# Kernel optimization log

Measured on AMD Instinct MI355X. Metric: run time of the kernel, lower is better.

Reference implementation:

```python
import jax, jax.numpy as jnp
import numpy as np

B, S, D, C = 1024, 200, 64, 256  # batch, max_seq_length_all, reshape_size, codebook_size


def setup_inputs() -> dict:
    key = jax.random.key(0)
    k1, k2, k3 = jax.random.split(key, 3)
    rq_item_embeddings = jax.random.normal(k1, (B, S, D), dtype=jnp.float32)
    labels = jax.random.randint(k2, (B, S), 0, C, dtype=jnp.int32)
    attention_mask = jax.random.randint(k3, (B, S), 0, 2, dtype=jnp.int32)
    return {
        "rq_item_embeddings": rq_item_embeddings,
        "labels": labels,
        "attention_mask": attention_mask,
    }


def reference(rq_item_embeddings, labels, attention_mask):
    # Batched version of the original per-sample loop:
    #   M[c, s] = 1 if labels[s] == c, masked by attention_mask[s]
    #   M <- L1-normalize over seq dim (divide each cluster row by its count)
    #   cluster_emb = M @ sample  (per-cluster mean of item embeddings)
    x = rq_item_embeddings  # [B, S, D]
    mask = attention_mask.astype(x.dtype)  # [B, S]
    # one-hot cluster assignment, [B, C, S]
    one_hot = (labels[:, None, :] == jnp.arange(C, dtype=labels.dtype)[None, :, None])
    cluster_mask = one_hot.astype(x.dtype) * mask[:, None, :]  # [B, C, S]
    counts = cluster_mask.sum(axis=-1)  # [B, C]  (== L1 norm of each row)
    inv = jnp.where(counts > 0, 1.0 / jnp.maximum(counts, 1.0), 0.0)  # [B, C]
    # normalized scatter matrix @ embeddings -> per-cluster mean, [B, C, D]
    cluster_emb = jnp.einsum('bcs,bsd->bcd', cluster_mask, x) * inv[:, :, None]
    return cluster_emb, cluster_mask.astype(jnp.int32)
```

## Files before the change

kernel.cpp:

```cpp
#include <hip/hip_runtime.h>

#define NB 1024
#define NS 200
#define ND 64
#define NC 256

typedef float v4f __attribute__((ext_vector_type(4)));

__global__ __launch_bounds__(256) void s3rec_mask_kernel(
    const int* __restrict__ labels,
    const int* __restrict__ amask,
    float* __restrict__ out_mask)
{
    __shared__ __align__(16) int s_lab[NS];

    const int bid = blockIdx.x;
    const int b   = bid >> 2;
    const int ct  = (bid & 3) << 6;
    const int t   = threadIdx.x;

    for (int i = t; i < NS; i += 256) {
        const int l = labels[b * NS + i];
        const int m = amask [b * NS + i];
        s_lab[i] = (m != 0) ? l : -1;
    }
    __syncthreads();

    const int4* lab4 = reinterpret_cast<const int4*>(s_lab);
    v4f* om4 = reinterpret_cast<v4f*>(out_mask + (size_t)b * (NC * NS)) + ct * 50;
    for (int i4 = t; i4 < 64 * 50; i4 += 256) {
        const int cl = i4 / 50;
        const int s4 = i4 - cl * 50;
        const int c  = ct + cl;
        const int4 L = lab4[s4];
        v4f v;
        v.x = (L.x == c) ? 1.0f : 0.0f;
        v.y = (L.y == c) ? 1.0f : 0.0f;
        v.z = (L.z == c) ? 1.0f : 0.0f;
        v.w = (L.w == c) ? 1.0f : 0.0f;
        om4[i4] = v;
    }
}

__global__ __launch_bounds__(256) void s3rec_emb_kernel(
    const float* __restrict__ x,
    const int*   __restrict__ labels,
    const int*   __restrict__ amask,
    float* __restrict__ out_emb)
{
    __shared__ __align__(16) float s_emb[NC * ND];
    __shared__ int   s_lab[NS];
    __shared__ float s_inv[NC];

    const int b = blockIdx.x;
    const int t = threadIdx.x;

    for (int i = t; i < NS; i += 256) {
        const int l = labels[b * NS + i];
        const int m = amask [b * NS + i];
        s_lab[i] = (m != 0) ? l : -1;
    }
    v4f* se4 = reinterpret_cast<v4f*>(s_emb);
    for (int i = t; i < (NC * ND) / 4; i += 256) {
        v4f z = {0.0f, 0.0f, 0.0f, 0.0f};
        se4[i] = z;
    }
    __syncthreads();

    const int lane = t & 63;
    const int w    = t >> 6;
    const float* xb = x + (size_t)b * NS * ND;
    for (int s = w; s < NS; s += 4) {
        const int c = s_lab[s];
        if (c >= 0) {
            atomicAdd(&s_emb[c * ND + lane], xb[s * ND + lane]);
        }
    }

    int cnt = 0;
    #pragma unroll 8
    for (int s = 0; s < NS; ++s) cnt += (s_lab[s] == t) ? 1 : 0;
    s_inv[t] = (cnt > 0) ? (1.0f / (float)cnt) : 0.0f;
    __syncthreads();

    v4f* oe4 = reinterpret_cast<v4f*>(out_emb + (size_t)b * (NC * ND));
    for (int i4 = t; i4 < (NC * ND) / 4; i4 += 256) {
        const float inv = s_inv[i4 >> 4];
        v4f v = se4[i4] * inv;
        oe4[i4] = v;
    }
}

extern "C" void kernel_launch(void* const* d_in, const int* in_sizes, int n_in,
                              void* d_out, int out_size, void* d_ws, size_t ws_size,
                              hipStream_t stream) {
    const float* x      = (const float*)d_in[0];
    const int*   labels = (const int*)  d_in[1];
    const int*   amask  = (const int*)  d_in[2];

    float* out_emb  = (float*)d_out;
    float* out_mask = out_emb + (size_t)NB * NC * ND;

    s3rec_mask_kernel<<<dim3(NB * 4), dim3(256), 0, stream>>>(labels, amask, out_mask);
    s3rec_emb_kernel <<<dim3(NB),     dim3(256), 0, stream>>>(x, labels, amask, out_emb);
}
```

Measured before the change: 369.0 us.

## Replace dense one-hot mask build with zero-fill plus scatter of ones

Builds the cluster mask by first zeroing the whole output with a grid-stride vector store kernel, then launching a small kernel that writes 1.0 at each valid (label, position). This drops the per-element compare work and shared-memory staging of the old mask kernel, keeping a pure streaming store. It adds a third kernel launch and a dependent scattered write pass. The count loop in the embedding kernel also now reads labels as int4 vectors.

Measured after the change: 362.0 us. Within noise of the previous version (-1.9%).

```diff
diff --git a/kernel.cpp b/kernel.cpp
--- a/kernel.cpp
+++ b/kernel.cpp
@@ -7,38 +7,27 @@
 
 typedef float v4f __attribute__((ext_vector_type(4)));
 
-__global__ __launch_bounds__(256) void s3rec_mask_kernel(
+__global__ __launch_bounds__(256) void s3rec_zero_mask(float* __restrict__ out_mask) {
+    v4f* p = reinterpret_cast<v4f*>(out_mask);
+    const v4f z = {0.0f, 0.0f, 0.0f, 0.0f};
+    const int n4 = (NB * NC * NS) / 4;
+    const int stride = gridDim.x * blockDim.x;
+    for (int i = blockIdx.x * blockDim.x + threadIdx.x; i < n4; i += stride)
+        p[i] = z;
+}
+
+__global__ __launch_bounds__(256) void s3rec_scatter_ones(
     const int* __restrict__ labels,
     const int* __restrict__ amask,
     float* __restrict__ out_mask)
 {
-    __shared__ __align__(16) int s_lab[NS];
-
-    const int bid = blockIdx.x;
-    const int b   = bid >> 2;
-    const int ct  = (bid & 3) << 6;
-    const int t   = threadIdx.x;
-
-    for (int i = t; i < NS; i += 256) {
-        const int l = labels[b * NS + i];
-        const int m = amask [b * NS + i];
-        s_lab[i] = (m != 0) ? l : -1;
-    }
-    __syncthreads();
-
-    const int4* lab4 = reinterpret_cast<const int4*>(s_lab);
-    v4f* om4 = reinterpret_cast<v4f*>(out_mask + (size_t)b * (NC * NS)) + ct * 50;
-    for (int i4 = t; i4 < 64 * 50; i4 += 256) {
-        const int cl = i4 / 50;
-        const int s4 = i4 - cl * 50;
-        const int c  = ct + cl;
-        const int4 L = lab4[s4];
-        v4f v;
-        v.x = (L.x == c) ? 1.0f : 0.0f;
-        v.y = (L.y == c) ? 1.0f : 0.0f;
-        v.z = (L.z == c) ? 1.0f : 0.0f;
-        v.w = (L.w == c) ? 1.0f : 0.0f;
-        om4[i4] = v;
+    const int b = blockIdx.x;
+    const int t = threadIdx.x;
+    if (t < NS) {
+        const int l = labels[b * NS + t];
+        const int m = amask [b * NS + t];
+        if (m != 0)
+            out_mask[(size_t)b * (NC * NS) + (size_t)l * NS + t] = 1.0f;
     }
 }
 
@@ -49,7 +38,7 @@
     float* __restrict__ out_emb)
 {
     __shared__ __align__(16) float s_emb[NC * ND];
-    __shared__ int   s_lab[NS];
+    __shared__ __align__(16) int   s_lab[NS];
     __shared__ float s_inv[NC];
 
     const int b = blockIdx.x;
@@ -77,9 +66,13 @@
         }
     }
 
+    const int4* lab4 = reinterpret_cast<const int4*>(s_lab);
     int cnt = 0;
-    #pragma unroll 8
-    for (int s = 0; s < NS; ++s) cnt += (s_lab[s] == t) ? 1 : 0;
+    #pragma unroll 10
+    for (int s4 = 0; s4 < NS / 4; ++s4) {
+        const int4 L = lab4[s4];
+        cnt += (L.x == t) + (L.y == t) + (L.z == t) + (L.w == t);
+    }
     s_inv[t] = (cnt > 0) ? (1.0f / (float)cnt) : 0.0f;
     __syncthreads();
 
@@ -101,6 +94,7 @@
     float* out_emb  = (float*)d_out;
     float* out_mask = out_emb + (size_t)NB * NC * ND;
 
-    s3rec_mask_kernel<<<dim3(NB * 4), dim3(256), 0, stream>>>(labels, amask, out_mask);
-    s3rec_emb_kernel <<<dim3(NB),     dim3(256), 0, stream>>>(x, labels, amask, out_emb);
+    s3rec_zero_mask   <<<dim3(4096), dim3(256), 0, stream>>>(out_mask);
+    s3rec_scatter_ones<<<dim3(NB),   dim3(256), 0, stream>>>(labels, amask, out_mask);
+    s3rec_emb_kernel  <<<dim3(NB),   dim3(256), 0, stream>>>(x, labels, amask, out_emb);
 }
```
